# Optimization experiments

Measured on AMD Instinct MI355X. Metric: run time of the kernel, lower is better.

Reference implementation:

```python
import jax, jax.numpy as jnp
import numpy as np
import math

NUM_SECTORS = 8
HIDDEN = 128
FEAT = 64
MAX_DIST = 10.0


def gru_last(x, Wih, Whh, bih, bhh):
    # PyTorch GRU (gate order r,z,n); x: (B,T,D) -> last hidden (B,H)
    B = x.shape[0]
    H = Whh.shape[1]
    xp = jnp.einsum('btd,gd->btg', x, Wih) + bih  # (B,T,3H)

    def step(h, xpt):
        hp = h @ Whh.T + bhh
        xr, xz, xn = jnp.split(xpt, 3, -1)
        hr, hz, hn = jnp.split(hp, 3, -1)
        r = jax.nn.sigmoid(xr + hr)
        z = jax.nn.sigmoid(xz + hz)
        n = jnp.tanh(xn + r * hn)
        h_new = (1.0 - z) * n + z * h
        return h_new, None

    h0 = jnp.zeros((B, H), x.dtype)
    hT, _ = jax.lax.scan(step, h0, jnp.swapaxes(xp, 0, 1))
    return hT


def setup_inputs() -> dict:
    key = jax.random.key(0)
    ks = iter(jax.random.split(key, 32))
    B, N, T = 2048, 64, 8
    H, Hn = HIDDEN, HIDDEN // 2
    s = 0.05

    def p(shape):
        return jax.random.normal(next(ks), shape, jnp.float32) * s

    inp = {
        'target_trajectory': jax.random.normal(next(ks), (B, T, 2), jnp.float32),
        'neighbor_trajectories': jax.random.normal(next(ks), (B, N, T, 2), jnp.float32),
        'relative_angles': jax.random.uniform(next(ks), (B, N), jnp.float32) * (2.0 * math.pi),
        'neighbor_mask': (jax.random.uniform(next(ks), (B, N)) > 0.2).astype(jnp.float32),
        # target GRU (H=128)
        'Wih_t': p((3 * H, 2)), 'Whh_t': p((3 * H, H)), 'bih_t': p((3 * H,)), 'bhh_t': p((3 * H,)),
        # neighbor GRU (H=64)
        'Wih_n': p((3 * Hn, 2)), 'Whh_n': p((3 * Hn, Hn)), 'bih_n': p((3 * Hn,)), 'bhh_n': p((3 * Hn,)),
        # sector encoder: 68 -> 128 -> 128
        'W1': p((H, 4 + Hn)), 'b1': p((H,)), 'W2': p((H, H)), 'b2': p((H,)),
        # fusion: 1152 -> 256 -> 128 -> 64
        'Wf1': p((2 * H, H + NUM_SECTORS * H)), 'bf1': p((2 * H,)),
        'Wf2': p((H, 2 * H)), 'bf2': p((H,)),
        'Wf3': p((FEAT, H)), 'bf3': p((FEAT,)),
        'ln_g': jnp.ones((FEAT,), jnp.float32), 'ln_b': jnp.zeros((FEAT,), jnp.float32),
    }
    return inp


def reference(target_trajectory, neighbor_trajectories, relative_angles, neighbor_mask,
              Wih_t, Whh_t, bih_t, bhh_t, Wih_n, Whh_n, bih_n, bhh_n,
              W1, b1, W2, b2, Wf1, bf1, Wf2, bf2, Wf3, bf3, ln_g, ln_b):
    B, N, T, D = neighbor_trajectories.shape
    S = NUM_SECTORS

    # trajectory encoders
    target_feature = gru_last(target_trajectory, Wih_t, Whh_t, bih_t, bhh_t)  # (B,128)
    nf = gru_last(neighbor_trajectories.reshape(B * N, T, D), Wih_n, Whh_n, bih_n, bhh_n)
    nf = nf.reshape(B, N, -1)  # (B,N,64)

    # geometry
    target_pos = target_trajectory[:, -1, :]                      # (B,2)
    npos = neighbor_trajectories[:, :, -1, :]                     # (B,N,2)
    dist = jnp.linalg.norm(npos - target_pos[:, None, :], axis=-1)  # (B,N)
    vel = neighbor_trajectories[:, :, -1, :] - neighbor_trajectories[:, :, -2, :]  # (B,N,2)

    # sector assignment (vectorized segment reduce over sectors)
    sector_size = 2.0 * math.pi / S
    sid = jnp.clip((relative_angles / sector_size).astype(jnp.int32), 0, S - 1)  # (B,N)
    valid = neighbor_mask > 0
    memb = ((sid[..., None] == jnp.arange(S)) & valid[..., None]).astype(dist.dtype)  # (B,N,S)

    count = memb.sum(1)                        # (B,S)
    nonempty = count > 0
    safe = jnp.maximum(count, 1.0)
    avg_d = jnp.where(nonempty, (dist[..., None] * memb).sum(1) / safe, 0.0)  # (B,S)
    avg_v = jnp.where(nonempty[..., None], jnp.einsum('bns,bnc->bsc', memb, vel) / safe[..., None], 0.0)

    w = jnp.exp(-dist / MAX_DIST)              # (B,N)
    wm = w[..., None] * memb                   # (B,N,S)
    wsum = wm.sum(1) + 1e-8                    # (B,S)
    wfeat = jnp.einsum('bns,bnh->bsh', wm, nf) / wsum[..., None]  # (B,S,64)

    sector_feats = jnp.concatenate([count[..., None], avg_d[..., None], avg_v, wfeat], axis=-1)  # (B,S,68)

    # sector encoder MLP (dropout off / eval)
    h = jax.nn.relu(sector_feats @ W1.T + b1)
    h = jax.nn.relu(h @ W2.T + b2)             # (B,S,128)
    enc = h.reshape(B, S * HIDDEN)

    combined = jnp.concatenate([target_feature, enc], axis=-1)  # (B,1152)
    f = jax.nn.relu(combined @ Wf1.T + bf1)
    f = jax.nn.relu(f @ Wf2.T + bf2)
    f = jax.nn.relu(f @ Wf3.T + bf3)           # (B,64)

    mu = f.mean(-1, keepdims=True)
    var = ((f - mu) ** 2).mean(-1, keepdims=True)
    return (f - mu) / jnp.sqrt(var + 1e-5) * ln_g + ln_b
```

## Files before the change

### kernel.cpp

```cpp
#include <hip/hip_runtime.h>

typedef __attribute__((ext_vector_type(8))) short short8;
typedef __attribute__((ext_vector_type(4))) float f32x4;

#define SGC (-1.44269504088896341f)
#define THC ( 2.88539008177792681f)

__device__ __forceinline__ unsigned short f2bf(float f){
  unsigned u = __float_as_uint(f);
  return (unsigned short)((u + 0x7fffu + ((u >> 16) & 1u)) >> 16);
}
__device__ __forceinline__ float bf2f(unsigned short b){
  return __uint_as_float(((unsigned)b) << 16);
}
__device__ __forceinline__ unsigned f2bf_cvt(float f){
  unsigned r;
  asm("v_cvt_pk_bf16_f32 %0, %1, %1" : "=v"(r) : "v"(f));
  return r;
}
__device__ __forceinline__ unsigned f2bf_pk(float lo, float hi){
  unsigned r;
  asm("v_cvt_pk_bf16_f32 %0, %1, %2" : "=v"(r) : "v"(lo), "v"(hi));
  return r;
}

__global__ __launch_bounds__(256) void k_prep(
    const float* __restrict__ Whh_t, const float* __restrict__ W1,
    const float* __restrict__ W2,    const float* __restrict__ Wf1,
    const float* __restrict__ Wf2,   const float* __restrict__ Wf3,
    const float* __restrict__ Whh_n, const float* __restrict__ Wih_n,
    const float* __restrict__ bih_n, const float* __restrict__ bhh_n,
    unsigned short* __restrict__ wgt)
{
  int i = blockIdx.x * 256 + threadIdx.x;
  if (i < 49152){
    int g = i >> 7;
    float s = (g < 256) ? SGC : THC;
    wgt[i] = f2bf(Whh_t[i] * s); return;
  }
  i -= 49152;
  if (i < 12288){ int r = i / 96, c = i % 96;
    wgt[49152 + i] = (c < 68) ? f2bf(W1[r*68 + c]) : (unsigned short)0; return; }
  i -= 12288;
  if (i < 16384){ wgt[61440 + i] = f2bf(W2[i]); return; }
  i -= 16384;
  if (i < 294912){ wgt[77824 + i] = f2bf(Wf1[i]); return; }
  i -= 294912;
  if (i < 32768){ wgt[372736 + i] = f2bf(Wf2[i]); return; }
  i -= 32768;
  if (i < 8192){ wgt[405504 + i] = f2bf(Wf3[i]); return; }
  i -= 8192;
  if (i < 12288){
    int g = i >> 6;
    float s = (g < 128) ? SGC : THC;
    wgt[413696 + i] = f2bf(Whh_n[i] * s); return;
  }
  i -= 12288;
  if (i < 1536){
    int t = i >> 7, rem = i & 127, cc = rem >> 3, j = rem & 7;
    float s = (t < 8) ? SGC : THC;
    int g = (t < 4) ? (t*16 + cc) : (t < 8) ? (64 + (t-4)*16 + cc) : (128 + (t-8)*16 + cc);
    float v = 0.f;
    if (j == 0) v = Wih_n[g*2]   * s;
    if (j == 1) v = Wih_n[g*2+1] * s;
    if (j == 2) v = ((t < 8) ? (bih_n[g] + bhh_n[g]) : bih_n[g]) * s;
    wgt[425984 + i] = f2bf(v); return;
  }
}

__global__ __launch_bounds__(256, 4) void k_gru_n(
    const float* __restrict__ ttraj, const float* __restrict__ ntraj,
    const float* __restrict__ rang,  const float* __restrict__ nmask,
    const float* __restrict__ bhh_n,
    const unsigned short* __restrict__ wgt,
    unsigned short* __restrict__ sf)
{
  __shared__ char smem[11264];
  const int tid = threadIdx.x;
  const int w = tid >> 6, u = (tid >> 4) & 3, c = tid & 15;
  const int b = blockIdx.x;
  const unsigned short* whhN_b = wgt + 413696;
  const unsigned short* wxg    = wgt + 425984;

  unsigned short* hbuf = (unsigned short*)smem;
  unsigned* xpk = (unsigned*)(smem + 9216);
  float* pool   = (float*)(smem + 9216);

  short8 Bh[6], Bx[3];
#pragma unroll
  for (int k = 0; k < 3; ++k){
    int nt = k*4 + w;
    Bh[k*2+0] = *(const short8*)&whhN_b[(nt*16 + c)*64 + u*8];
    Bh[k*2+1] = *(const short8*)&whhN_b[(nt*16 + c)*64 + 32 + u*8];
    Bx[k]     = *(const short8*)&wxg[nt*128 + c*8];
  }
  const float bh_ = bhh_n[128 + w*16 + c] * THC;

  {
    float4 v = ((const float4*)(ntraj + (size_t)b * 1024))[tid];
    int n = tid >> 2, p = (tid & 3) * 2;
    xpk[p*64 + n]     = f2bf_pk(v.x, v.y);
    xpk[(p+1)*64 + n] = f2bf_pk(v.z, v.w);
  }
  __syncthreads();

  float hcur[4][4];
#pragma unroll
  for (int sg=0; sg<4; ++sg)
#pragma unroll
    for (int q=0; q<4; ++q) hcur[sg][q] = 0.0f;

  const f32x4 zz = {0.f,0.f,0.f,0.f};

#pragma unroll 1
  for (int st = 0; st < 8; ++st){
    short8 a0s[4], a1s[4];
    unsigned xv[4];
#pragma unroll
    for (int sg = 0; sg < 4; ++sg){
      xv[sg] = xpk[st*64 + sg*16 + c];
      if (st > 0){
        a0s[sg] = *(short8*)&hbuf[(sg*16 + c)*72 + u*8];
        a1s[sg] = *(short8*)&hbuf[(sg*16 + c)*72 + 32 + u*8];
      }
    }
    __syncthreads();

#pragma unroll
    for (int sg = 0; sg < 4; ++sg){
      union { unsigned ui[4]; short8 s8; } a2u;
      a2u.ui[0] = (u == 0) ? xv[sg] : 0u;
      a2u.ui[1] = (u == 0) ? 0x3F80u : 0u;
      a2u.ui[2] = 0u; a2u.ui[3] = 0u;
      short8 a2 = a2u.s8;

      f32x4 aR = __builtin_amdgcn_mfma_f32_16x16x32_bf16(a2, Bx[0], zz, 0,0,0);
      f32x4 aZ = __builtin_amdgcn_mfma_f32_16x16x32_bf16(a2, Bx[1], zz, 0,0,0);
      f32x4 aX = __builtin_amdgcn_mfma_f32_16x16x32_bf16(a2, Bx[2], zz, 0,0,0);
      f32x4 aN = zz;
      if (st > 0){
        aR = __builtin_amdgcn_mfma_f32_16x16x32_bf16(a0s[sg], Bh[0], aR, 0,0,0);
        aR = __builtin_amdgcn_mfma_f32_16x16x32_bf16(a1s[sg], Bh[1], aR, 0,0,0);
        aZ = __builtin_amdgcn_mfma_f32_16x16x32_bf16(a0s[sg], Bh[2], aZ, 0,0,0);
        aZ = __builtin_amdgcn_mfma_f32_16x16x32_bf16(a1s[sg], Bh[3], aZ, 0,0,0);
        aN = __builtin_amdgcn_mfma_f32_16x16x32_bf16(a0s[sg], Bh[4], aN, 0,0,0);
        aN = __builtin_amdgcn_mfma_f32_16x16x32_bf16(a1s[sg], Bh[5], aN, 0,0,0);
      }
#pragma unroll
      for (int q = 0; q < 4; ++q){
        float r = __builtin_amdgcn_rcpf(1.0f + __builtin_amdgcn_exp2f(aR[q]));
        float z = __builtin_amdgcn_rcpf(1.0f + __builtin_amdgcn_exp2f(aZ[q]));
        float hn = aN[q] + bh_;
        float pn = __builtin_fmaf(r, hn, aX[q]);
        float E = __builtin_amdgcn_exp2f(pn);
        float n = __builtin_fmaf(-2.0f, __builtin_amdgcn_rcpf(E + 1.0f), 1.0f);
        float hnew = __builtin_fmaf(z, hcur[sg][q] - n, n);
        hcur[sg][q] = hnew;
        hbuf[(sg*16 + u*4 + q)*72 + w*16 + c] = (unsigned short)f2bf_cvt(hnew);
      }
    }
    __syncthreads();
  }

  if (tid < 64){
    int n = tid;
    const float* nb = ntraj + (size_t)b*1024 + n*16;
    float px = nb[14], py = nb[15];
    float vx = px - nb[12], vy = py - nb[13];
    float m   = nmask[(size_t)b*64 + n];
    float ang = rang[(size_t)b*64 + n];
    float tx = ttraj[(size_t)b*16 + 14], ty = ttraj[(size_t)b*16 + 15];
    float dx = px - tx, dy = py - ty;
    float dist = __builtin_amdgcn_sqrtf(dx*dx + dy*dy);
    int sid = (int)(ang / 0.78539816339744830962f);
    sid = sid < 0 ? 0 : (sid > 7 ? 7 : sid);
    bool valid = m > 0.0f;
    float wv = valid ? __builtin_amdgcn_exp2f(dist * -0.14426950408889634f) : 0.0f;
    pool[n]       = valid ? dist : 0.0f;
    pool[64 + n]  = valid ? vx   : 0.0f;
    pool[128 + n] = valid ? vy   : 0.0f;
    pool[192 + n] = wv;
    pool[256 + n] = valid ? (float)sid : -1.0f;
  }
  __syncthreads();
  if (tid < 8){
    int s = tid;
    float cnt=0.f, sd=0.f, sx=0.f, sy=0.f, sw=0.f;
#pragma unroll 4
    for (int n=0; n<64; ++n){
      if (pool[256+n] == (float)s){
        cnt += 1.f; sd += pool[n]; sx += pool[64+n]; sy += pool[128+n]; sw += pool[192+n];
      }
    }
    float inv = (cnt > 0.f) ? __builtin_amdgcn_rcpf(cnt) : 0.f;
    pool[320 + s] = cnt;
    pool[328 + s] = sd * inv;
    pool[336 + s] = sx * inv;
    pool[344 + s] = sy * inv;
    pool[352 + s] = __builtin_amdgcn_rcpf(sw + 1e-8f);
  }
  __syncthreads();
#pragma unroll
  for (int rep = 0; rep < 2; ++rep){
    int p = tid + rep*256;
    int s = p >> 6, h = p & 63;
    float fs = (float)s;
    float a = 0.f;
#pragma unroll 4
    for (int n = 0; n < 64; ++n){
      float wmv = (pool[256+n] == fs) ? pool[192+n] : 0.f;
      float nf  = bf2f(hbuf[n*72 + h]);
      a += wmv * nf;
    }
    sf[((size_t)b*8 + s)*96 + 4 + h] = (unsigned short)f2bf_cvt(a * pool[352+s]);
  }
  if (tid < 32){
    int s = tid >> 2, cc = tid & 3;
    sf[((size_t)b*8 + s)*96 + cc] = (unsigned short)f2bf_cvt(pool[320 + cc*8 + s]);
  }
  if (tid < 224){
    int s = tid / 28, cc = 68 + tid % 28;
    sf[((size_t)b*8 + s)*96 + cc] = 0;
  }
}

__global__ __launch_bounds__(256) void k_gru_t(
    const float* __restrict__ ttraj,
    const float* __restrict__ Wih_t, const float* __restrict__ bih_t, const float* __restrict__ bhh_t,
    const unsigned short* __restrict__ wgt,
    unsigned short* __restrict__ combined)
{
  __shared__ char smem[9728];
  const int tid = threadIdx.x, w = tid >> 6, u = (tid >> 4) & 3, c = tid & 15;
  unsigned short* hb0 = (unsigned short*)smem;
  unsigned short* hb1 = (unsigned short*)(smem + 4352);
  float* xs = (float*)(smem + 8704);

  xs[tid] = ttraj[(size_t)blockIdx.x*256 + tid];

  int ntg[6];
  ntg[0] = 2*w; ntg[1] = 2*w+1;
  ntg[2] = 8+2*w; ntg[3] = 9+2*w;
  ntg[4] = 16+2*w; ntg[5] = 17+2*w;

  short8 Bf[6][4];
#pragma unroll
  for (int lt2 = 0; lt2 < 6; ++lt2){
    const unsigned short* wp = wgt + (ntg[lt2]*16 + c)*128 + u*8;
#pragma unroll
    for (int kk = 0; kk < 4; ++kk)
      Bf[lt2][kk] = *(const short8*)(wp + kk*32);
  }

  float Wr0[2],Wr1[2],BR[2],Wz0[2],Wz1[2],BZ[2],Wn0[2],Wn1[2],BI[2],BH[2];
#pragma unroll
  for (int gt = 0; gt < 2; ++gt){
    int g = w*32 + gt*16 + c;
    Wr0[gt]=Wih_t[g*2]*SGC;        Wr1[gt]=Wih_t[g*2+1]*SGC;        BR[gt]=(bih_t[g]+bhh_t[g])*SGC;
    Wz0[gt]=Wih_t[(128+g)*2]*SGC;  Wz1[gt]=Wih_t[(128+g)*2+1]*SGC;  BZ[gt]=(bih_t[128+g]+bhh_t[128+g])*SGC;
    Wn0[gt]=Wih_t[(256+g)*2]*THC;  Wn1[gt]=Wih_t[(256+g)*2+1]*THC;  BI[gt]=bih_t[256+g]*THC; BH[gt]=bhh_t[256+g]*THC;
  }
  float hcur[2][4];
#pragma unroll
  for (int gt=0; gt<2; ++gt)
#pragma unroll
    for (int q=0; q<4; ++q) hcur[gt][q] = 0.0f;
  __syncthreads();

#pragma unroll 1
  for (int st = 0; st < 8; ++st){
    unsigned short* rbuf = (st & 1) ? hb0 : hb1;
    unsigned short* wbuf = (st & 1) ? hb1 : hb0;
    f32x4 acc[6];
    if (st > 0){
      short8 a0 = *(short8*)&rbuf[c*136 + u*8];
      short8 a1 = *(short8*)&rbuf[c*136 + 32 + u*8];
      short8 a2 = *(short8*)&rbuf[c*136 + 64 + u*8];
      short8 a3 = *(short8*)&rbuf[c*136 + 96 + u*8];
#pragma unroll
      for (int lt2 = 0; lt2 < 6; ++lt2){
        f32x4 t = {0.f,0.f,0.f,0.f};
        t = __builtin_amdgcn_mfma_f32_16x16x32_bf16(a0, Bf[lt2][0], t, 0,0,0);
        t = __builtin_amdgcn_mfma_f32_16x16x32_bf16(a1, Bf[lt2][1], t, 0,0,0);
        t = __builtin_amdgcn_mfma_f32_16x16x32_bf16(a2, Bf[lt2][2], t, 0,0,0);
        acc[lt2] = __builtin_amdgcn_mfma_f32_16x16x32_bf16(a3, Bf[lt2][3], t, 0,0,0);
      }
    } else {
#pragma unroll
      for (int lt2 = 0; lt2 < 6; ++lt2) acc[lt2] = (f32x4){0.f,0.f,0.f,0.f};
    }
#pragma unroll
    for (int gt = 0; gt < 2; ++gt){
#pragma unroll
      for (int q = 0; q < 4; ++q){
        int sq = u*4 + q;
        float x0 = xs[sq*16 + st*2], x1 = xs[sq*16 + st*2 + 1];
        float rp = __builtin_fmaf(Wr0[gt], x0, __builtin_fmaf(Wr1[gt], x1, acc[gt][q] + BR[gt]));
        float zp = __builtin_fmaf(Wz0[gt], x0, __builtin_fmaf(Wz1[gt], x1, acc[2+gt][q] + BZ[gt]));
        float r = __builtin_amdgcn_rcpf(1.0f + __builtin_amdgcn_exp2f(rp));
        float z = __builtin_amdgcn_rcpf(1.0f + __builtin_amdgcn_exp2f(zp));
        float hnv = acc[4+gt][q] + BH[gt];
        float pn = __builtin_fmaf(Wn0[gt], x0, __builtin_fmaf(Wn1[gt], x1, __builtin_fmaf(r, hnv, BI[gt])));
        float E = __builtin_amdgcn_exp2f(pn);
        float n = __builtin_fmaf(-2.0f, __builtin_amdgcn_rcpf(E + 1.0f), 1.0f);
        float hnew = __builtin_fmaf(z, hcur[gt][q] - n, n);
        hcur[gt][q] = hnew;
        if (st < 7){
          wbuf[sq*136 + w*32 + gt*16 + c] = (unsigned short)f2bf_cvt(hnew);
        } else {
          int row = blockIdx.x*16 + sq;
          combined[(size_t)row*1152 + w*32 + gt*16 + c] = (unsigned short)f2bf_cvt(hnew);
        }
      }
    }
    if (st < 7) __syncthreads();
  }
}

__global__ __launch_bounds__(256) void k_mlp12(
    const unsigned short* __restrict__ sf,
    const unsigned short* __restrict__ wgt,
    const float* __restrict__ b1, const float* __restrict__ b2,
    unsigned short* __restrict__ combined)
{
  __shared__ char smem[18432];
  unsigned short* hb = (unsigned short*)smem + (threadIdx.x >> 6) * 2176;
  float* b1s = (float*)(smem + 17408);
  float* b2s = b1s + 128;
  const unsigned short* w1b = wgt + 49152;
  const unsigned short* w2b = wgt + 61440;
  const int tid = threadIdx.x, w = tid >> 6, u = (tid >> 4) & 3, c = tid & 15;
  if (tid < 128){ b1s[tid] = b1[tid]; b2s[tid] = b2[tid]; }
  __syncthreads();
  const int rowb = blockIdx.x * 64 + w * 16;

  f32x4 acc[8];
#pragma unroll
  for (int nt=0; nt<8; ++nt) acc[nt] = (f32x4){0.f,0.f,0.f,0.f};
#pragma unroll
  for (int kc=0; kc<3; ++kc){
    short8 a = *(const short8*)&sf[(size_t)(rowb + c)*96 + kc*32 + u*8];
#pragma unroll
    for (int nt=0; nt<8; ++nt){
      short8 bb = *(const short8*)&w1b[(nt*16+c)*96 + kc*32 + u*8];
      acc[nt] = __builtin_amdgcn_mfma_f32_16x16x32_bf16(a, bb, acc[nt], 0,0,0);
    }
  }
#pragma unroll
  for (int nt=0; nt<8; ++nt){
    float bias = b1s[nt*16+c];
#pragma unroll
    for (int q=0; q<4; ++q){
      float v = acc[nt][q] + bias; v = v > 0.f ? v : 0.f;
      hb[(u*4+q)*136 + nt*16 + c] = (unsigned short)f2bf_cvt(v);
    }
  }
  f32x4 acc2[8];
#pragma unroll
  for (int nt=0; nt<8; ++nt) acc2[nt] = (f32x4){0.f,0.f,0.f,0.f};
#pragma unroll
  for (int kc=0; kc<4; ++kc){
    short8 a = *(short8*)&hb[c*136 + kc*32 + u*8];
#pragma unroll
    for (int nt=0; nt<8; ++nt){
      short8 bb = *(const short8*)&w2b[(nt*16+c)*128 + kc*32 + u*8];
      acc2[nt] = __builtin_amdgcn_mfma_f32_16x16x32_bf16(a, bb, acc2[nt], 0,0,0);
    }
  }
#pragma unroll
  for (int nt=0; nt<8; ++nt){
    float bias = b2s[nt*16+c];
#pragma unroll
    for (int q=0; q<4; ++q){
      float v = acc2[nt][q] + bias; v = v > 0.f ? v : 0.f;
      int r = rowb + u*4 + q;
      combined[(size_t)(r >> 3)*1152 + 128 + (r & 7)*128 + nt*16 + c] = (unsigned short)f2bf_cvt(v);
    }
  }
}

__global__ __launch_bounds__(256) void k_head(
    const unsigned short* __restrict__ combined,
    const unsigned short* __restrict__ wgt,
    const float* __restrict__ bf1, const float* __restrict__ bf2, const float* __restrict__ bf3,
    const float* __restrict__ lng, const float* __restrict__ lnb,
    float* __restrict__ out)
{
  __shared__ char smem[15104];
  const int tid = threadIdx.x, w = tid >> 6, u = (tid >> 4) & 3, c = tid & 15;
  unsigned short* f1b = (unsigned short*)smem;
  unsigned short* f2b = (unsigned short*)(smem + 8448);
  float* bf1s = (float*)(smem + 12800); float* bf2s = (float*)(smem + 13824);
  float* bf3s = (float*)(smem + 14336);
  float* lngs = (float*)(smem + 14592); float* lnbs = (float*)(smem + 14848);
  const unsigned short* wf1b = wgt + 77824;
  const unsigned short* wf2b = wgt + 372736;
  const unsigned short* wf3b = wgt + 405504;
  bf1s[tid] = bf1[tid];
  if (tid < 128) bf2s[tid] = bf2[tid];
  if (tid < 64){ bf3s[tid] = bf3[tid]; lngs[tid] = lng[tid]; lnbs[tid] = lnb[tid]; }
  __syncthreads();
  const int rowb = blockIdx.x * 16;

  f32x4 acc[4];
#pragma unroll
  for (int i=0; i<4; ++i) acc[i] = (f32x4){0.f,0.f,0.f,0.f};
#pragma unroll 4
  for (int kc=0; kc<36; ++kc){
    short8 a = *(const short8*)&combined[(size_t)(rowb + c)*1152 + kc*32 + u*8];
#pragma unroll
    for (int i=0; i<4; ++i){
      int nt = w*4 + i;
      short8 bb = *(const short8*)&wf1b[(size_t)(nt*16+c)*1152 + kc*32 + u*8];
      acc[i] = __builtin_amdgcn_mfma_f32_16x16x32_bf16(a, bb, acc[i], 0,0,0);
    }
  }
#pragma unroll
  for (int i=0; i<4; ++i){
    int nt = w*4 + i;
    float bias = bf1s[nt*16+c];
#pragma unroll
    for (int q=0; q<4; ++q){
      float v = acc[i][q] + bias; v = v > 0.f ? v : 0.f;
      f1b[(u*4+q)*264 + nt*16 + c] = (unsigned short)f2bf_cvt(v);
    }
  }
  __syncthreads();

  f32x4 acc2[2];
#pragma unroll
  for (int i=0; i<2; ++i) acc2[i] = (f32x4){0.f,0.f,0.f,0.f};
#pragma unroll
  for (int kc=0; kc<8; ++kc){
    short8 a = *(short8*)&f1b[c*264 + kc*32 + u*8];
#pragma unroll
    for (int i=0; i<2; ++i){
      int nt = w*2 + i;
      short8 bb = *(const short8*)&wf2b[(nt*16+c)*256 + kc*32 + u*8];
      acc2[i] = __builtin_amdgcn_mfma_f32_16x16x32_bf16(a, bb, acc2[i], 0,0,0);
    }
  }
#pragma unroll
  for (int i=0; i<2; ++i){
    int nt = w*2 + i;
    float bias = bf2s[nt*16+c];
#pragma unroll
    for (int q=0; q<4; ++q){
      float v = acc2[i][q] + bias; v = v > 0.f ? v : 0.f;
      f2b[(u*4+q)*136 + nt*16 + c] = (unsigned short)f2bf_cvt(v);
    }
  }
  __syncthreads();

  f32x4 acc3[4];
#pragma unroll
  for (int nt=0; nt<4; ++nt) acc3[nt] = (f32x4){0.f,0.f,0.f,0.f};
#pragma unroll
  for (int kc=0; kc<4; ++kc){
    short8 a = *(short8*)&f2b[c*136 + kc*32 + u*8];
#pragma unroll
    for (int nt=0; nt<4; ++nt){
      short8 bb = *(const short8*)&wf3b[(nt*16+c)*128 + kc*32 + u*8];
      acc3[nt] = __builtin_amdgcn_mfma_f32_16x16x32_bf16(a, bb, acc3[nt], 0,0,0);
    }
  }
  if (w == 0){
    float v[4][4];
#pragma unroll
    for (int nt=0; nt<4; ++nt){
      float bias = bf3s[nt*16+c];
#pragma unroll
      for (int q=0; q<4; ++q){
        float t = acc3[nt][q] + bias; v[nt][q] = t > 0.f ? t : 0.f;
      }
    }
#pragma unroll
    for (int q=0; q<4; ++q){
      float p = v[0][q] + v[1][q] + v[2][q] + v[3][q];
      p += __shfl_xor(p, 1); p += __shfl_xor(p, 2); p += __shfl_xor(p, 4); p += __shfl_xor(p, 8);
      float mu = p * 0.015625f;
      float d0 = v[0][q]-mu, d1 = v[1][q]-mu, d2 = v[2][q]-mu, d3 = v[3][q]-mu;
      float p2 = d0*d0 + d1*d1 + d2*d2 + d3*d3;
      p2 += __shfl_xor(p2, 1); p2 += __shfl_xor(p2, 2); p2 += __shfl_xor(p2, 4); p2 += __shfl_xor(p2, 8);
      float rstd = __builtin_amdgcn_rsqf(p2 * 0.015625f + 1e-5f);
      int row = rowb + u*4 + q;
#pragma unroll
      for (int nt=0; nt<4; ++nt){
        int col = nt*16 + c;
        out[(size_t)row*64 + col] = (v[nt][q] - mu) * rstd * lngs[col] + lnbs[col];
      }
    }
  }
}

extern "C" void kernel_launch(void* const* d_in, const int* in_sizes, int n_in,
                              void* d_out, int out_size, void* d_ws, size_t ws_size,
                              hipStream_t stream)
{
  const float* ttraj = (const float*)d_in[0];
  const float* ntraj = (const float*)d_in[1];
  const float* rang  = (const float*)d_in[2];
  const float* nmask = (const float*)d_in[3];
  const float* Wih_t = (const float*)d_in[4];
  const float* Whh_t = (const float*)d_in[5];
  const float* bih_t = (const float*)d_in[6];
  const float* bhh_t = (const float*)d_in[7];
  const float* Wih_n = (const float*)d_in[8];
  const float* Whh_n = (const float*)d_in[9];
  const float* bih_n = (const float*)d_in[10];
  const float* bhh_n = (const float*)d_in[11];
  const float* W1  = (const float*)d_in[12];
  const float* b1  = (const float*)d_in[13];
  const float* W2  = (const float*)d_in[14];
  const float* b2  = (const float*)d_in[15];
  const float* Wf1 = (const float*)d_in[16];
  const float* bf1 = (const float*)d_in[17];
  const float* Wf2 = (const float*)d_in[18];
  const float* bf2 = (const float*)d_in[19];
  const float* Wf3 = (const float*)d_in[20];
  const float* bf3 = (const float*)d_in[21];
  const float* lng = (const float*)d_in[22];
  const float* lnb = (const float*)d_in[23];

  char* ws = (char*)d_ws;
  unsigned short* combined = (unsigned short*)ws;
  unsigned short* sf       = (unsigned short*)(ws + 5242880);
  unsigned short* wgt      = (unsigned short*)(ws + 8388608);

  hipLaunchKernelGGL(k_prep, dim3(1670), dim3(256), 0, stream,
                     Whh_t, W1, W2, Wf1, Wf2, Wf3, Whh_n, Wih_n, bih_n, bhh_n, wgt);
  hipLaunchKernelGGL(k_gru_n, dim3(2048), dim3(256), 0, stream,
                     ttraj, ntraj, rang, nmask, bhh_n, wgt, sf);
  hipLaunchKernelGGL(k_gru_t, dim3(128), dim3(256), 0, stream,
                     ttraj, Wih_t, bih_t, bhh_t, wgt, combined);
  hipLaunchKernelGGL(k_mlp12, dim3(256), dim3(256), 0, stream, sf, wgt, b1, b2, combined);
  hipLaunchKernelGGL(k_head, dim3(128), dim3(256), 0, stream,
                     combined, wgt, bf1, bf2, bf3, lng, lnb, (float*)d_out);
}
```

Before: 138.2 us.

## Merge weight prep and both GRU kernels into one heterogeneous launch

Combines the weight-conversion kernel, the neighbor GRU and the target GRU into one kernel, with branches chosen by block index. The GRU blocks now convert their recurrent weights from fp32 on the fly instead of reading pre-converted bf16, which removes their dependency on the prep kernel. This cuts two launches and the serialization between them. In exchange, every neighbor block re-reads and converts fp32 weights, and the merged kernel drops the occupancy hint the neighbor GRU had.

```diff
diff --git a/kernel.cpp b/kernel.cpp
--- a/kernel.cpp
+++ b/kernel.cpp
@@ -24,296 +24,284 @@
   return r;
 }
 
-__global__ __launch_bounds__(256) void k_prep(
-    const float* __restrict__ Whh_t, const float* __restrict__ W1,
-    const float* __restrict__ W2,    const float* __restrict__ Wf1,
-    const float* __restrict__ Wf2,   const float* __restrict__ Wf3,
-    const float* __restrict__ Whh_n, const float* __restrict__ Wih_n,
-    const float* __restrict__ bih_n, const float* __restrict__ bhh_n,
-    unsigned short* __restrict__ wgt)
-{
-  int i = blockIdx.x * 256 + threadIdx.x;
-  if (i < 49152){
-    int g = i >> 7;
-    float s = (g < 256) ? SGC : THC;
-    wgt[i] = f2bf(Whh_t[i] * s); return;
-  }
-  i -= 49152;
-  if (i < 12288){ int r = i / 96, c = i % 96;
-    wgt[49152 + i] = (c < 68) ? f2bf(W1[r*68 + c]) : (unsigned short)0; return; }
-  i -= 12288;
-  if (i < 16384){ wgt[61440 + i] = f2bf(W2[i]); return; }
-  i -= 16384;
-  if (i < 294912){ wgt[77824 + i] = f2bf(Wf1[i]); return; }
-  i -= 294912;
-  if (i < 32768){ wgt[372736 + i] = f2bf(Wf2[i]); return; }
-  i -= 32768;
-  if (i < 8192){ wgt[405504 + i] = f2bf(Wf3[i]); return; }
-  i -= 8192;
-  if (i < 12288){
-    int g = i >> 6;
-    float s = (g < 128) ? SGC : THC;
-    wgt[413696 + i] = f2bf(Whh_n[i] * s); return;
-  }
-  i -= 12288;
-  if (i < 1536){
-    int t = i >> 7, rem = i & 127, cc = rem >> 3, j = rem & 7;
-    float s = (t < 8) ? SGC : THC;
-    int g = (t < 4) ? (t*16 + cc) : (t < 8) ? (64 + (t-4)*16 + cc) : (128 + (t-8)*16 + cc);
-    float v = 0.f;
-    if (j == 0) v = Wih_n[g*2]   * s;
-    if (j == 1) v = Wih_n[g*2+1] * s;
-    if (j == 2) v = ((t < 8) ? (bih_n[g] + bhh_n[g]) : bih_n[g]) * s;
-    wgt[425984 + i] = f2bf(v); return;
-  }
-}
-
-__global__ __launch_bounds__(256, 4) void k_gru_n(
+
+__global__ __launch_bounds__(256) void k_main(
     const float* __restrict__ ttraj, const float* __restrict__ ntraj,
     const float* __restrict__ rang,  const float* __restrict__ nmask,
-    const float* __restrict__ bhh_n,
-    const unsigned short* __restrict__ wgt,
-    unsigned short* __restrict__ sf)
+    const float* __restrict__ Wih_n, const float* __restrict__ bih_n,
+    const float* __restrict__ bhh_n, const float* __restrict__ Whh_n,
+    const float* __restrict__ Wih_t, const float* __restrict__ bih_t,
+    const float* __restrict__ bhh_t, const float* __restrict__ Whh_t,
+    const float* __restrict__ W1,    const float* __restrict__ W2,
+    const float* __restrict__ Wf1,   const float* __restrict__ Wf2,
+    const float* __restrict__ Wf3,
+    unsigned short* __restrict__ wgt,
+    unsigned short* __restrict__ sf,
+    unsigned short* __restrict__ combined)
 {
   __shared__ char smem[11264];
   const int tid = threadIdx.x;
   const int w = tid >> 6, u = (tid >> 4) & 3, c = tid & 15;
-  const int b = blockIdx.x;
-  const unsigned short* whhN_b = wgt + 413696;
-  const unsigned short* wxg    = wgt + 425984;
-
-  unsigned short* hbuf = (unsigned short*)smem;
-  unsigned* xpk = (unsigned*)(smem + 9216);
-  float* pool   = (float*)(smem + 9216);
-
-  short8 Bh[6], Bx[3];
-#pragma unroll
-  for (int k = 0; k < 3; ++k){
-    int nt = k*4 + w;
-    Bh[k*2+0] = *(const short8*)&whhN_b[(nt*16 + c)*64 + u*8];
-    Bh[k*2+1] = *(const short8*)&whhN_b[(nt*16 + c)*64 + 32 + u*8];
-    Bx[k]     = *(const short8*)&wxg[nt*128 + c*8];
-  }
-  const float bh_ = bhh_n[128 + w*16 + c] * THC;
-
-  {
-    float4 v = ((const float4*)(ntraj + (size_t)b * 1024))[tid];
-    int n = tid >> 2, p = (tid & 3) * 2;
-    xpk[p*64 + n]     = f2bf_pk(v.x, v.y);
-    xpk[(p+1)*64 + n] = f2bf_pk(v.z, v.w);
-  }
-  __syncthreads();
-
-  float hcur[4][4];
-#pragma unroll
-  for (int sg=0; sg<4; ++sg)
-#pragma unroll
-    for (int q=0; q<4; ++q) hcur[sg][q] = 0.0f;
-
   const f32x4 zz = {0.f,0.f,0.f,0.f};
 
+  if (blockIdx.x >= 1552){
+    const int b = blockIdx.x - 1552;
+    unsigned short* hbuf = (unsigned short*)smem;
+    unsigned* xpk = (unsigned*)(smem + 9216);
+    float* pool   = (float*)(smem + 9216);
+
+    short8 Bh[6], Bx[3];
+#pragma unroll
+    for (int k = 0; k < 3; ++k){
+      float s = (k < 2) ? SGC : THC;
+      const float* src = Whh_n + ((size_t)((k*4 + w)*16 + c))*64;
+#pragma unroll
+      for (int h = 0; h < 2; ++h){
+        const float* p = src + h*32 + u*8;
+        union { unsigned ui[4]; short8 s8; } t;
+#pragma unroll
+        for (int j = 0; j < 4; ++j) t.ui[j] = f2bf_pk(p[2*j]*s, p[2*j+1]*s);
+        Bh[k*2+h] = t.s8;
+      }
+      int g = k*64 + w*16 + c;
+      float bsum = ((k < 2) ? (bih_n[g] + bhh_n[g]) : bih_n[g]);
+      union { unsigned ui[4]; short8 s8; } tx;
+      tx.ui[0] = f2bf_pk(Wih_n[g*2]*s, Wih_n[g*2+1]*s);
+      tx.ui[1] = f2bf_pk(bsum*s, 0.f);
+      tx.ui[2] = 0u; tx.ui[3] = 0u;
+      Bx[k] = tx.s8;
+    }
+    const float bh_ = bhh_n[128 + w*16 + c] * THC;
+
+    {
+      float4 v = ((const float4*)(ntraj + (size_t)b * 1024))[tid];
+      int n = tid >> 2, p = (tid & 3) * 2;
+      xpk[p*64 + n]     = f2bf_pk(v.x, v.y);
+      xpk[(p+1)*64 + n] = f2bf_pk(v.z, v.w);
+    }
+    __syncthreads();
+
+    float hcur[4][4];
+#pragma unroll
+    for (int sg=0; sg<4; ++sg)
+#pragma unroll
+      for (int q=0; q<4; ++q) hcur[sg][q] = 0.0f;
+
 #pragma unroll 1
-  for (int st = 0; st < 8; ++st){
-    short8 a0s[4], a1s[4];
-    unsigned xv[4];
-#pragma unroll
-    for (int sg = 0; sg < 4; ++sg){
-      xv[sg] = xpk[st*64 + sg*16 + c];
+    for (int st = 0; st < 8; ++st){
+      short8 a0s[4], a1s[4];
+      unsigned xv[4];
+#pragma unroll
+      for (int sg = 0; sg < 4; ++sg){
+        xv[sg] = xpk[st*64 + sg*16 + c];
+        if (st > 0){
+          a0s[sg] = *(short8*)&hbuf[(sg*16 + c)*72 + u*8];
+          a1s[sg] = *(short8*)&hbuf[(sg*16 + c)*72 + 32 + u*8];
+        }
+      }
+      __syncthreads();
+
+#pragma unroll
+      for (int sg = 0; sg < 4; ++sg){
+        union { unsigned ui[4]; short8 s8; } a2u;
+        a2u.ui[0] = (u == 0) ? xv[sg] : 0u;
+        a2u.ui[1] = (u == 0) ? 0x3F80u : 0u;
+        a2u.ui[2] = 0u; a2u.ui[3] = 0u;
+        short8 a2 = a2u.s8;
+
+        f32x4 aR = __builtin_amdgcn_mfma_f32_16x16x32_bf16(a2, Bx[0], zz, 0,0,0);
+        f32x4 aZ = __builtin_amdgcn_mfma_f32_16x16x32_bf16(a2, Bx[1], zz, 0,0,0);
+        f32x4 aX = __builtin_amdgcn_mfma_f32_16x16x32_bf16(a2, Bx[2], zz, 0,0,0);
+        f32x4 aN = zz;
+        if (st > 0){
+          aR = __builtin_amdgcn_mfma_f32_16x16x32_bf16(a0s[sg], Bh[0], aR, 0,0,0);
+          aR = __builtin_amdgcn_mfma_f32_16x16x32_bf16(a1s[sg], Bh[1], aR, 0,0,0);
+          aZ = __builtin_amdgcn_mfma_f32_16x16x32_bf16(a0s[sg], Bh[2], aZ, 0,0,0);
+          aZ = __builtin_amdgcn_mfma_f32_16x16x32_bf16(a1s[sg], Bh[3], aZ, 0,0,0);
+          aN = __builtin_amdgcn_mfma_f32_16x16x32_bf16(a0s[sg], Bh[4], aN, 0,0,0);
+          aN = __builtin_amdgcn_mfma_f32_16x16x32_bf16(a1s[sg], Bh[5], aN, 0,0,0);
+        }
+#pragma unroll
+        for (int q = 0; q < 4; ++q){
+          float r = __builtin_amdgcn_rcpf(1.0f + __builtin_amdgcn_exp2f(aR[q]));
+          float z = __builtin_amdgcn_rcpf(1.0f + __builtin_amdgcn_exp2f(aZ[q]));
+          float hn = aN[q] + bh_;
+          float pn = __builtin_fmaf(r, hn, aX[q]);
+          float E = __builtin_amdgcn_exp2f(pn);
+          float n = __builtin_fmaf(-2.0f, __builtin_amdgcn_rcpf(E + 1.0f), 1.0f);
+          float hnew = __builtin_fmaf(z, hcur[sg][q] - n, n);
+          hcur[sg][q] = hnew;
+          hbuf[(sg*16 + u*4 + q)*72 + w*16 + c] = (unsigned short)f2bf_cvt(hnew);
+        }
+      }
+      __syncthreads();
+    }
+
+    if (tid < 64){
+      int n = tid;
+      const float* nb = ntraj + (size_t)b*1024 + n*16;
+      float px = nb[14], py = nb[15];
+      float vx = px - nb[12], vy = py - nb[13];
+      float m   = nmask[(size_t)b*64 + n];
+      float ang = rang[(size_t)b*64 + n];
+      float tx = ttraj[(size_t)b*16 + 14], ty = ttraj[(size_t)b*16 + 15];
+      float dx = px - tx, dy = py - ty;
+      float dist = __builtin_amdgcn_sqrtf(dx*dx + dy*dy);
+      int sid = (int)(ang / 0.78539816339744830962f);
+      sid = sid < 0 ? 0 : (sid > 7 ? 7 : sid);
+      bool valid = m > 0.0f;
+      float wv = valid ? __builtin_amdgcn_exp2f(dist * -0.14426950408889634f) : 0.0f;
+      pool[n]       = valid ? dist : 0.0f;
+      pool[64 + n]  = valid ? vx   : 0.0f;
+      pool[128 + n] = valid ? vy   : 0.0f;
+      pool[192 + n] = wv;
+      pool[256 + n] = valid ? (float)sid : -1.0f;
+    }
+    __syncthreads();
+    if (tid < 8){
+      int s = tid;
+      float cnt=0.f, sd=0.f, sx=0.f, sy=0.f, sw=0.f;
+#pragma unroll 4
+      for (int n=0; n<64; ++n){
+        if (pool[256+n] == (float)s){
+          cnt += 1.f; sd += pool[n]; sx += pool[64+n]; sy += pool[128+n]; sw += pool[192+n];
+        }
+      }
+      float inv = (cnt > 0.f) ? __builtin_amdgcn_rcpf(cnt) : 0.f;
+      pool[320 + s] = cnt;
+      pool[328 + s] = sd * inv;
+      pool[336 + s] = sx * inv;
+      pool[344 + s] = sy * inv;
+      pool[352 + s] = __builtin_amdgcn_rcpf(sw + 1e-8f);
+    }
+    __syncthreads();
+#pragma unroll
+    for (int rep = 0; rep < 2; ++rep){
+      int p = tid + rep*256;
+      int s = p >> 6, h = p & 63;
+      float fs = (float)s;
+      float a = 0.f;
+#pragma unroll 4
+      for (int n = 0; n < 64; ++n){
+        float wmv = (pool[256+n] == fs) ? pool[192+n] : 0.f;
+        float nf  = bf2f(hbuf[n*72 + h]);
+        a += wmv * nf;
+      }
+      sf[((size_t)b*8 + s)*96 + 4 + h] = (unsigned short)f2bf_cvt(a * pool[352+s]);
+    }
+    if (tid < 32){
+      int s = tid >> 2, cc = tid & 3;
+      sf[((size_t)b*8 + s)*96 + cc] = (unsigned short)f2bf_cvt(pool[320 + cc*8 + s]);
+    }
+    if (tid < 224){
+      int s = tid / 28, cc = 68 + tid % 28;
+      sf[((size_t)b*8 + s)*96 + cc] = 0;
+    }
+
+  } else if (blockIdx.x >= 128){
+    int i = (blockIdx.x - 128) * 256 + tid;
+    if (i < 12288){ int r = i / 96, cc = i % 96;
+      wgt[i] = (cc < 68) ? f2bf(W1[r*68 + cc]) : (unsigned short)0; return; }
+    i -= 12288;
+    if (i < 16384){ wgt[12288 + i] = f2bf(W2[i]); return; }
+    i -= 16384;
+    if (i < 294912){ wgt[28672 + i] = f2bf(Wf1[i]); return; }
+    i -= 294912;
+    if (i < 32768){ wgt[323584 + i] = f2bf(Wf2[i]); return; }
+    i -= 32768;
+    if (i < 8192){ wgt[356352 + i] = f2bf(Wf3[i]); return; }
+
+  } else {
+    const int bt = blockIdx.x;
+    unsigned short* hb0 = (unsigned short*)smem;
+    unsigned short* hb1 = (unsigned short*)(smem + 4352);
+    float* xs = (float*)(smem + 8704);
+
+    xs[tid] = ttraj[(size_t)bt*256 + tid];
+
+    int ntg[6];
+    ntg[0] = 2*w; ntg[1] = 2*w+1;
+    ntg[2] = 8+2*w; ntg[3] = 9+2*w;
+    ntg[4] = 16+2*w; ntg[5] = 17+2*w;
+
+    short8 Bf[6][4];
+#pragma unroll
+    for (int lt2 = 0; lt2 < 6; ++lt2){
+      float s = (lt2 < 4) ? SGC : THC;
+      const float* wp = Whh_t + (size_t)(ntg[lt2]*16 + c)*128 + u*8;
+#pragma unroll
+      for (int kk = 0; kk < 4; ++kk){
+        const float* p = wp + kk*32;
+        union { unsigned ui[4]; short8 s8; } t;
+#pragma unroll
+        for (int j = 0; j < 4; ++j) t.ui[j] = f2bf_pk(p[2*j]*s, p[2*j+1]*s);
+        Bf[lt2][kk] = t.s8;
+      }
+    }
+
+    float Wr0[2],Wr1[2],BR[2],Wz0[2],Wz1[2],BZ[2],Wn0[2],Wn1[2],BI[2],BH[2];
+#pragma unroll
+    for (int gt = 0; gt < 2; ++gt){
+      int g = w*32 + gt*16 + c;
+      Wr0[gt]=Wih_t[g*2]*SGC;        Wr1[gt]=Wih_t[g*2+1]*SGC;        BR[gt]=(bih_t[g]+bhh_t[g])*SGC;
+      Wz0[gt]=Wih_t[(128+g)*2]*SGC;  Wz1[gt]=Wih_t[(128+g)*2+1]*SGC;  BZ[gt]=(bih_t[128+g]+bhh_t[128+g])*SGC;
+      Wn0[gt]=Wih_t[(256+g)*2]*THC;  Wn1[gt]=Wih_t[(256+g)*2+1]*THC;  BI[gt]=bih_t[256+g]*THC; BH[gt]=bhh_t[256+g]*THC;
+    }
+    float hcur[2][4];
+#pragma unroll
+    for (int gt=0; gt<2; ++gt)
+#pragma unroll
+      for (int q=0; q<4; ++q) hcur[gt][q] = 0.0f;
+    __syncthreads();
+
+#pragma unroll 1
+    for (int st = 0; st < 8; ++st){
+      unsigned short* rbuf = (st & 1) ? hb0 : hb1;
+      unsigned short* wbuf = (st & 1) ? hb1 : hb0;
+      f32x4 acc[6];
       if (st > 0){
-        a0s[sg] = *(short8*)&hbuf[(sg*16 + c)*72 + u*8];
-        a1s[sg] = *(short8*)&hbuf[(sg*16 + c)*72 + 32 + u*8];
-      }
-    }
-    __syncthreads();
-
-#pragma unroll
-    for (int sg = 0; sg < 4; ++sg){
-      union { unsigned ui[4]; short8 s8; } a2u;
-      a2u.ui[0] = (u == 0) ? xv[sg] : 0u;
-      a2u.ui[1] = (u == 0) ? 0x3F80u : 0u;
-      a2u.ui[2] = 0u; a2u.ui[3] = 0u;
-      short8 a2 = a2u.s8;
-
-      f32x4 aR = __builtin_amdgcn_mfma_f32_16x16x32_bf16(a2, Bx[0], zz, 0,0,0);
-      f32x4 aZ = __builtin_amdgcn_mfma_f32_16x16x32_bf16(a2, Bx[1], zz, 0,0,0);
-      f32x4 aX = __builtin_amdgcn_mfma_f32_16x16x32_bf16(a2, Bx[2], zz, 0,0,0);
-      f32x4 aN = zz;
-      if (st > 0){
-        aR = __builtin_amdgcn_mfma_f32_16x16x32_bf16(a0s[sg], Bh[0], aR, 0,0,0);
-        aR = __builtin_amdgcn_mfma_f32_16x16x32_bf16(a1s[sg], Bh[1], aR, 0,0,0);
-        aZ = __builtin_amdgcn_mfma_f32_16x16x32_bf16(a0s[sg], Bh[2], aZ, 0,0,0);
-        aZ = __builtin_amdgcn_mfma_f32_16x16x32_bf16(a1s[sg], Bh[3], aZ, 0,0,0);
-        aN = __builtin_amdgcn_mfma_f32_16x16x32_bf16(a0s[sg], Bh[4], aN, 0,0,0);
-        aN = __builtin_amdgcn_mfma_f32_16x16x32_bf16(a1s[sg], Bh[5], aN, 0,0,0);
-      }
-#pragma unroll
-      for (int q = 0; q < 4; ++q){
-        float r = __builtin_amdgcn_rcpf(1.0f + __builtin_amdgcn_exp2f(aR[q]));
-        float z = __builtin_amdgcn_rcpf(1.0f + __builtin_amdgcn_exp2f(aZ[q]));
-        float hn = aN[q] + bh_;
-        float pn = __builtin_fmaf(r, hn, aX[q]);
-        float E = __builtin_amdgcn_exp2f(pn);
-        float n = __builtin_fmaf(-2.0f, __builtin_amdgcn_rcpf(E + 1.0f), 1.0f);
-        float hnew = __builtin_fmaf(z, hcur[sg][q] - n, n);
-        hcur[sg][q] = hnew;
-        hbuf[(sg*16 + u*4 + q)*72 + w*16 + c] = (unsigned short)f2bf_cvt(hnew);
-      }
-    }
-    __syncthreads();
-  }
-
-  if (tid < 64){
-    int n = tid;
-    const float* nb = ntraj + (size_t)b*1024 + n*16;
-    float px = nb[14], py = nb[15];
-    float vx = px - nb[12], vy = py - nb[13];
-    float m   = nmask[(size_t)b*64 + n];
-    float ang = rang[(size_t)b*64 + n];
-    float tx = ttraj[(size_t)b*16 + 14], ty = ttraj[(size_t)b*16 + 15];
-    float dx = px - tx, dy = py - ty;
-    float dist = __builtin_amdgcn_sqrtf(dx*dx + dy*dy);
-    int sid = (int)(ang / 0.78539816339744830962f);
-    sid = sid < 0 ? 0 : (sid > 7 ? 7 : sid);
-    bool valid = m > 0.0f;
-    float wv = valid ? __builtin_amdgcn_exp2f(dist * -0.14426950408889634f) : 0.0f;
-    pool[n]       = valid ? dist : 0.0f;
-    pool[64 + n]  = valid ? vx   : 0.0f;
-    pool[128 + n] = valid ? vy   : 0.0f;
-    pool[192 + n] = wv;
-    pool[256 + n] = valid ? (float)sid : -1.0f;
-  }
-  __syncthreads();
-  if (tid < 8){
-    int s = tid;
-    float cnt=0.f, sd=0.f, sx=0.f, sy=0.f, sw=0.f;
-#pragma unroll 4
-    for (int n=0; n<64; ++n){
-      if (pool[256+n] == (float)s){
-        cnt += 1.f; sd += pool[n]; sx += pool[64+n]; sy += pool[128+n]; sw += pool[192+n];
-      }
-    }
-    float inv = (cnt > 0.f) ? __builtin_amdgcn_rcpf(cnt) : 0.f;
-    pool[320 + s] = cnt;
-    pool[328 + s] = sd * inv;
-    pool[336 + s] = sx * inv;
-    pool[344 + s] = sy * inv;
-    pool[352 + s] = __builtin_amdgcn_rcpf(sw + 1e-8f);
-  }
-  __syncthreads();
-#pragma unroll
-  for (int rep = 0; rep < 2; ++rep){
-    int p = tid + rep*256;
-    int s = p >> 6, h = p & 63;
-    float fs = (float)s;
-    float a = 0.f;
-#pragma unroll 4
-    for (int n = 0; n < 64; ++n){
-      float wmv = (pool[256+n] == fs) ? pool[192+n] : 0.f;
-      float nf  = bf2f(hbuf[n*72 + h]);
-      a += wmv * nf;
-    }
-    sf[((size_t)b*8 + s)*96 + 4 + h] = (unsigned short)f2bf_cvt(a * pool[352+s]);
-  }
-  if (tid < 32){
-    int s = tid >> 2, cc = tid & 3;
-    sf[((size_t)b*8 + s)*96 + cc] = (unsigned short)f2bf_cvt(pool[320 + cc*8 + s]);
-  }
-  if (tid < 224){
-    int s = tid / 28, cc = 68 + tid % 28;
-    sf[((size_t)b*8 + s)*96 + cc] = 0;
-  }
-}
-
-__global__ __launch_bounds__(256) void k_gru_t(
-    const float* __restrict__ ttraj,
-    const float* __restrict__ Wih_t, const float* __restrict__ bih_t, const float* __restrict__ bhh_t,
-    const unsigned short* __restrict__ wgt,
-    unsigned short* __restrict__ combined)
-{
-  __shared__ char smem[9728];
-  const int tid = threadIdx.x, w = tid >> 6, u = (tid >> 4) & 3, c = tid & 15;
-  unsigned short* hb0 = (unsigned short*)smem;
-  unsigned short* hb1 = (unsigned short*)(smem + 4352);
-  float* xs = (float*)(smem + 8704);
-
-  xs[tid] = ttraj[(size_t)blockIdx.x*256 + tid];
-
-  int ntg[6];
-  ntg[0] = 2*w; ntg[1] = 2*w+1;
-  ntg[2] = 8+2*w; ntg[3] = 9+2*w;
-  ntg[4] = 16+2*w; ntg[5] = 17+2*w;
-
-  short8 Bf[6][4];
-#pragma unroll
-  for (int lt2 = 0; lt2 < 6; ++lt2){
-    const unsigned short* wp = wgt + (ntg[lt2]*16 + c)*128 + u*8;
-#pragma unroll
-    for (int kk = 0; kk < 4; ++kk)
-      Bf[lt2][kk] = *(const short8*)(wp + kk*32);
-  }
-
-  float Wr0[2],Wr1[2],BR[2],Wz0[2],Wz1[2],BZ[2],Wn0[2],Wn1[2],BI[2],BH[2];
-#pragma unroll
-  for (int gt = 0; gt < 2; ++gt){
-    int g = w*32 + gt*16 + c;
-    Wr0[gt]=Wih_t[g*2]*SGC;        Wr1[gt]=Wih_t[g*2+1]*SGC;        BR[gt]=(bih_t[g]+bhh_t[g])*SGC;
-    Wz0[gt]=Wih_t[(128+g)*2]*SGC;  Wz1[gt]=Wih_t[(128+g)*2+1]*SGC;  BZ[gt]=(bih_t[128+g]+bhh_t[128+g])*SGC;
-    Wn0[gt]=Wih_t[(256+g)*2]*THC;  Wn1[gt]=Wih_t[(256+g)*2+1]*THC;  BI[gt]=bih_t[256+g]*THC; BH[gt]=bhh_t[256+g]*THC;
-  }
-  float hcur[2][4];
-#pragma unroll
-  for (int gt=0; gt<2; ++gt)
-#pragma unroll
-    for (int q=0; q<4; ++q) hcur[gt][q] = 0.0f;
-  __syncthreads();
-
-#pragma unroll 1
-  for (int st = 0; st < 8; ++st){
-    unsigned short* rbuf = (st & 1) ? hb0 : hb1;
-    unsigned short* wbuf = (st & 1) ? hb1 : hb0;
-    f32x4 acc[6];
-    if (st > 0){
-      short8 a0 = *(short8*)&rbuf[c*136 + u*8];
-      short8 a1 = *(short8*)&rbuf[c*136 + 32 + u*8];
-      short8 a2 = *(short8*)&rbuf[c*136 + 64 + u*8];
-      short8 a3 = *(short8*)&rbuf[c*136 + 96 + u*8];
-#pragma unroll
-      for (int lt2 = 0; lt2 < 6; ++lt2){
-        f32x4 t = {0.f,0.f,0.f,0.f};
-        t = __builtin_amdgcn_mfma_f32_16x16x32_bf16(a0, Bf[lt2][0], t, 0,0,0);
-        t = __builtin_amdgcn_mfma_f32_16x16x32_bf16(a1, Bf[lt2][1], t, 0,0,0);
-        t = __builtin_amdgcn_mfma_f32_16x16x32_bf16(a2, Bf[lt2][2], t, 0,0,0);
-        acc[lt2] = __builtin_amdgcn_mfma_f32_16x16x32_bf16(a3, Bf[lt2][3], t, 0,0,0);
-      }
-    } else {
-#pragma unroll
-      for (int lt2 = 0; lt2 < 6; ++lt2) acc[lt2] = (f32x4){0.f,0.f,0.f,0.f};
-    }
-#pragma unroll
-    for (int gt = 0; gt < 2; ++gt){
-#pragma unroll
-      for (int q = 0; q < 4; ++q){
-        int sq = u*4 + q;
-        float x0 = xs[sq*16 + st*2], x1 = xs[sq*16 + st*2 + 1];
-        float rp = __builtin_fmaf(Wr0[gt], x0, __builtin_fmaf(Wr1[gt], x1, acc[gt][q] + BR[gt]));
-        float zp = __builtin_fmaf(Wz0[gt], x0, __builtin_fmaf(Wz1[gt], x1, acc[2+gt][q] + BZ[gt]));
-        float r = __builtin_amdgcn_rcpf(1.0f + __builtin_amdgcn_exp2f(rp));
-        float z = __builtin_amdgcn_rcpf(1.0f + __builtin_amdgcn_exp2f(zp));
-        float hnv = acc[4+gt][q] + BH[gt];
-        float pn = __builtin_fmaf(Wn0[gt], x0, __builtin_fmaf(Wn1[gt], x1, __builtin_fmaf(r, hnv, BI[gt])));
-        float E = __builtin_amdgcn_exp2f(pn);
-        float n = __builtin_fmaf(-2.0f, __builtin_amdgcn_rcpf(E + 1.0f), 1.0f);
-        float hnew = __builtin_fmaf(z, hcur[gt][q] - n, n);
-        hcur[gt][q] = hnew;
-        if (st < 7){
-          wbuf[sq*136 + w*32 + gt*16 + c] = (unsigned short)f2bf_cvt(hnew);
-        } else {
-          int row = blockIdx.x*16 + sq;
-          combined[(size_t)row*1152 + w*32 + gt*16 + c] = (unsigned short)f2bf_cvt(hnew);
+        short8 a0 = *(short8*)&rbuf[c*136 + u*8];
+        short8 a1 = *(short8*)&rbuf[c*136 + 32 + u*8];
+        short8 a2 = *(short8*)&rbuf[c*136 + 64 + u*8];
+        short8 a3 = *(short8*)&rbuf[c*136 + 96 + u*8];
+#pragma unroll
+        for (int lt2 = 0; lt2 < 6; ++lt2){
+          f32x4 t = {0.f,0.f,0.f,0.f};
+          t = __builtin_amdgcn_mfma_f32_16x16x32_bf16(a0, Bf[lt2][0], t, 0,0,0);
+          t = __builtin_amdgcn_mfma_f32_16x16x32_bf16(a1, Bf[lt2][1], t, 0,0,0);
+          t = __builtin_amdgcn_mfma_f32_16x16x32_bf16(a2, Bf[lt2][2], t, 0,0,0);
+          acc[lt2] = __builtin_amdgcn_mfma_f32_16x16x32_bf16(a3, Bf[lt2][3], t, 0,0,0);
         }
-      }
-    }
-    if (st < 7) __syncthreads();
+      } else {
+#pragma unroll
+        for (int lt2 = 0; lt2 < 6; ++lt2) acc[lt2] = (f32x4){0.f,0.f,0.f,0.f};
+      }
+#pragma unroll
+      for (int gt = 0; gt < 2; ++gt){
+#pragma unroll
+        for (int q = 0; q < 4; ++q){
+          int sq = u*4 + q;
+          float x0 = xs[sq*16 + st*2], x1 = xs[sq*16 + st*2 + 1];
+          float rp = __builtin_fmaf(Wr0[gt], x0, __builtin_fmaf(Wr1[gt], x1, acc[gt][q] + BR[gt]));
+          float zp = __builtin_fmaf(Wz0[gt], x0, __builtin_fmaf(Wz1[gt], x1, acc[2+gt][q] + BZ[gt]));
+          float r = __builtin_amdgcn_rcpf(1.0f + __builtin_amdgcn_exp2f(rp));
+          float z = __builtin_amdgcn_rcpf(1.0f + __builtin_amdgcn_exp2f(zp));
+          float hnv = acc[4+gt][q] + BH[gt];
+          float pn = __builtin_fmaf(Wn0[gt], x0, __builtin_fmaf(Wn1[gt], x1, __builtin_fmaf(r, hnv, BI[gt])));
+          float E = __builtin_amdgcn_exp2f(pn);
+          float n = __builtin_fmaf(-2.0f, __builtin_amdgcn_rcpf(E + 1.0f), 1.0f);
+          float hnew = __builtin_fmaf(z, hcur[gt][q] - n, n);
+          hcur[gt][q] = hnew;
+          if (st < 7){
+            wbuf[sq*136 + w*32 + gt*16 + c] = (unsigned short)f2bf_cvt(hnew);
+          } else {
+            int row = bt*16 + sq;
+            combined[(size_t)row*1152 + w*32 + gt*16 + c] = (unsigned short)f2bf_cvt(hnew);
+          }
+        }
+      }
+      if (st < 7) __syncthreads();
+    }
   }
 }
 
@@ -327,8 +315,8 @@
   unsigned short* hb = (unsigned short*)smem + (threadIdx.x >> 6) * 2176;
   float* b1s = (float*)(smem + 17408);
   float* b2s = b1s + 128;
-  const unsigned short* w1b = wgt + 49152;
-  const unsigned short* w2b = wgt + 61440;
+  const unsigned short* w1b = wgt;
+  const unsigned short* w2b = wgt + 12288;
   const int tid = threadIdx.x, w = tid >> 6, u = (tid >> 4) & 3, c = tid & 15;
   if (tid < 128){ b1s[tid] = b1[tid]; b2s[tid] = b2[tid]; }
   __syncthreads();
@@ -393,9 +381,9 @@
   float* bf1s = (float*)(smem + 12800); float* bf2s = (float*)(smem + 13824);
   float* bf3s = (float*)(smem + 14336);
   float* lngs = (float*)(smem + 14592); float* lnbs = (float*)(smem + 14848);
-  const unsigned short* wf1b = wgt + 77824;
-  const unsigned short* wf2b = wgt + 372736;
-  const unsigned short* wf3b = wgt + 405504;
+  const unsigned short* wf1b = wgt + 28672;
+  const unsigned short* wf2b = wgt + 323584;
+  const unsigned short* wf3b = wgt + 356352;
   bf1s[tid] = bf1[tid];
   if (tid < 128) bf2s[tid] = bf2[tid];
   if (tid < 64){ bf3s[tid] = bf3[tid]; lngs[tid] = lng[tid]; lnbs[tid] = lnb[tid]; }
@@ -527,12 +515,12 @@
   unsigned short* sf       = (unsigned short*)(ws + 5242880);
   unsigned short* wgt      = (unsigned short*)(ws + 8388608);
 
-  hipLaunchKernelGGL(k_prep, dim3(1670), dim3(256), 0, stream,
-                     Whh_t, W1, W2, Wf1, Wf2, Wf3, Whh_n, Wih_n, bih_n, bhh_n, wgt);
-  hipLaunchKernelGGL(k_gru_n, dim3(2048), dim3(256), 0, stream,
-                     ttraj, ntraj, rang, nmask, bhh_n, wgt, sf);
-  hipLaunchKernelGGL(k_gru_t, dim3(128), dim3(256), 0, stream,
-                     ttraj, Wih_t, bih_t, bhh_t, wgt, combined);
+  hipLaunchKernelGGL(k_main, dim3(3600), dim3(256), 0, stream,
+                     ttraj, ntraj, rang, nmask,
+                     Wih_n, bih_n, bhh_n, Whh_n,
+                     Wih_t, bih_t, bhh_t, Whh_t,
+                     W1, W2, Wf1, Wf2, Wf3,
+                     wgt, sf, combined);
   hipLaunchKernelGGL(k_mlp12, dim3(256), dim3(256), 0, stream, sf, wgt, b1, b2, combined);
   hipLaunchKernelGGL(k_head, dim3(128), dim3(256), 0, stream,
                      combined, wgt, bf1, bf2, bf3, lng, lnb, (float*)d_out);
```

After: 168.5 us. 21.9% more time.
